# Optimization experiments

Hardware: AMD Instinct MI355X
Metric: run time of the kernel (lower is better)

The kernel has to match this reference:

```python
import jax, jax.numpy as jnp
import numpy as np

B, S, D, H = 4, 2048, 1024, 16
DH = D // H


def setup_inputs() -> dict:
    key = jax.random.key(0)
    ks = jax.random.split(key, 12)
    s = 0.02
    inp = {
        "q": jax.random.normal(ks[0], (B, S, D), jnp.float32),
        "k": jax.random.normal(ks[1], (B, S, D), jnp.float32),
        "v": jax.random.normal(ks[2], (B, S, D), jnp.float32),
        # causal mask, broadcastable over batch and heads (mask==0 -> -1e9)
        "mask": jnp.tril(jnp.ones((S, S), jnp.int32))[None, None, :, :],
        "wq": jax.random.normal(ks[3], (D, D), jnp.float32) * s,
        "bq": jnp.zeros((D,), jnp.float32),
        "wk": jax.random.normal(ks[4], (D, D), jnp.float32) * s,
        "bk": jnp.zeros((D,), jnp.float32),
        "wv": jax.random.normal(ks[5], (D, D), jnp.float32) * s,
        "bv": jnp.zeros((D,), jnp.float32),
        "wo": jax.random.normal(ks[6], (D, D), jnp.float32) * s,
        "bo": jnp.zeros((D,), jnp.float32),
    }
    return inp


def reference(q, k, v, mask, wq, bq, wk, bk, wv, bv, wo, bo):
    # linear projections (torch Linear: x @ W^T + b)
    qh = (q @ wq.T + bq).reshape(B, S, H, DH).transpose(0, 2, 1, 3)  # [B,H,S,DH]
    kh = (k @ wk.T + bk).reshape(B, S, H, DH).transpose(0, 2, 1, 3)
    vh = (v @ wv.T + bv).reshape(B, S, H, DH).transpose(0, 2, 1, 3)
    scale = 1.0 / jnp.sqrt(jnp.float32(DH))
    score = jnp.einsum("bhqd,bhkd->bhqk", qh, kh) * scale  # [B,H,S,S]
    score = jnp.where(mask == 0, jnp.float32(-1e9), score)
    attn = jax.nn.softmax(score, axis=-1)
    ctx = jnp.einsum("bhqk,bhkd->bhqd", attn, vh)  # [B,H,S,DH]
    ctx = ctx.transpose(0, 2, 1, 3).reshape(B, S, D)
    return ctx @ wo.T + bo
```

## Files before the change

kernel.cpp:

```cpp
#include <hip/hip_runtime.h>
#include <hip/hip_bf16.h>

#define NB 4
#define NS 2048
#define ND 1024
#define NH 16
#define NDH 64
#define E_ 8388608
#define W_ 1048576

typedef __attribute__((ext_vector_type(8))) __bf16 bf16x8;
typedef __attribute__((ext_vector_type(4))) float f32x4;
typedef __attribute__((ext_vector_type(2))) unsigned int u32x2;
typedef unsigned short us16;
typedef unsigned int u32;

__device__ __forceinline__ unsigned short f2bf(float f) {
  union { float f; unsigned u; } v; v.f = f;
  unsigned r = v.u + 0x7FFFu + ((v.u >> 16) & 1u);
  return (unsigned short)(r >> 16);
}

typedef const __attribute__((address_space(1))) unsigned int* gas_t;
typedef __attribute__((address_space(3))) unsigned int* las_t;
__device__ __forceinline__ void gl2lds16(const void* g, void* l) {
  __builtin_amdgcn_global_load_lds((gas_t)g, (las_t)l, 16, 0, 0);
}

__global__ __launch_bounds__(256) void conv_bf16(
    const float* __restrict__ q, const float* __restrict__ k, const float* __restrict__ v,
    const float* __restrict__ wq, const float* __restrict__ wk, const float* __restrict__ wv,
    const float* __restrict__ wo,
    us16* __restrict__ qb, us16* __restrict__ kb, us16* __restrict__ vb,
    us16* __restrict__ wqb, us16* __restrict__ wkb, us16* __restrict__ wvb,
    us16* __restrict__ wob)
{
  int b = blockIdx.x;
  int seg, off;
  if (b < 24576) { seg = b >> 13; off = b & 8191; }
  else { b -= 24576; seg = 3 + (b >> 10); off = b & 1023; }
  const float* s; us16* d;
  switch (seg) {
    case 0: s = q;  d = qb;  break;
    case 1: s = k;  d = kb;  break;
    case 2: s = v;  d = vb;  break;
    case 3: s = wq; d = wqb; break;
    case 4: s = wk; d = wkb; break;
    case 5: s = wv; d = wvb; break;
    default: s = wo; d = wob; break;
  }
  size_t idx = ((size_t)off * 256 + threadIdx.x) * 4;
  float4 f = *(const float4*)(s + idx);
  ushort4 u;
  u.x = f2bf(f.x); u.y = f2bf(f.y); u.z = f2bf(f.z); u.w = f2bf(f.w);
  *(ushort4*)(d + idx) = u;
}

__global__ __launch_bounds__(256, 3) void gemm_proj3(
    const us16* __restrict__ A0, const us16* __restrict__ A1, const us16* __restrict__ A2,
    const us16* __restrict__ W0, const us16* __restrict__ W1, const us16* __restrict__ W2,
    const float* __restrict__ b0, const float* __restrict__ b1, const float* __restrict__ b2,
    us16* __restrict__ o0, us16* __restrict__ o1, us16* __restrict__ o2,
    float qscale, int s0, int s1, int s2)
{
  const int seg = (blockIdx.z == 0) ? s0 : (blockIdx.z == 1) ? s1 : s2;
  const us16* A  = (blockIdx.z == 0) ? A0 : (blockIdx.z == 1) ? A1 : A2;
  const us16* Wt = (blockIdx.z == 0) ? W0 : (blockIdx.z == 1) ? W1 : W2;
  const float* bias = (blockIdx.z == 0) ? b0 : (blockIdx.z == 1) ? b1 : b2;
  us16* out = (blockIdx.z == 0) ? o0 : (blockIdx.z == 1) ? o1 : o2;
  const float scale = (seg == 0) ? qscale : 1.0f;

  __shared__ us16 As[128][64];
  __shared__ us16 Bs[128][64];
  const int tid = threadIdx.x;
  const int lane = tid & 63;
  const int w = tid >> 6;
  const int l15 = lane & 15, quad = lane >> 4;
  const int sw = l15 & 7;
  const int rowBase = blockIdx.x * 128, colBase = blockIdx.y * 128;
  const int srow = w * 32 + (lane >> 3);
  const int cu = (lane & 7) ^ ((lane >> 3) & 7);
  const us16* ga = A  + (size_t)(rowBase + srow) * ND + cu * 8;
  const us16* gb = Wt + (size_t)(colBase + srow) * ND + cu * 8;
  const int wr = (w >> 1) * 64, wc = (w & 1) * 64;

  f32x4 acc[4][4] = {};
  for (int kt = 0; kt < ND; kt += 64) {
    __syncthreads();
    #pragma unroll
    for (int c = 0; c < 4; ++c) {
      gl2lds16(ga + kt + c * 8 * ND, &As[w * 32 + c * 8][0]);
      gl2lds16(gb + kt + c * 8 * ND, &Bs[w * 32 + c * 8][0]);
    }
    __syncthreads();
    #pragma unroll
    for (int ks = 0; ks < 2; ++ks) {
      bf16x8 af[4], bfr[4];
      #pragma unroll
      for (int i = 0; i < 4; ++i)
        af[i]  = *(const bf16x8*)&As[wr + i * 16 + l15][((ks * 4 + quad) ^ sw) * 8];
      #pragma unroll
      for (int j = 0; j < 4; ++j)
        bfr[j] = *(const bf16x8*)&Bs[wc + j * 16 + l15][((ks * 4 + quad) ^ sw) * 8];
      #pragma unroll
      for (int i = 0; i < 4; ++i)
        #pragma unroll
        for (int j = 0; j < 4; ++j)
          acc[i][j] = __builtin_amdgcn_mfma_f32_16x16x32_bf16(af[i], bfr[j], acc[i][j], 0, 0, 0);
    }
  }

  if (seg < 2) {
    #pragma unroll
    for (int i = 0; i < 4; ++i) {
      #pragma unroll
      for (int j = 0; j < 4; ++j) {
        int colg = colBase + wc + j * 16 + l15;
        float bval = bias[colg];
        #pragma unroll
        for (int r = 0; r < 4; ++r) {
          int rowg = rowBase + wr + i * 16 + quad * 4 + r;
          out[(size_t)rowg * ND + colg] = f2bf((acc[i][j][r] + bval) * scale);
        }
      }
    }
  } else {
    #pragma unroll
    for (int i = 0; i < 4; ++i) {
      #pragma unroll
      for (int j = 0; j < 4; ++j) {
        int colg = colBase + wc + j * 16 + l15;
        float bval = bias[colg];
        int h_ = colg >> 6, d_ = colg & 63;
        int rowg0 = rowBase + wr + i * 16 + quad * 4;
        int b_ = rowg0 >> 11, sr0 = rowg0 & (NS - 1);
        ushort4 vv;
        vv.x = f2bf(acc[i][j][0] + bval);
        vv.y = f2bf(acc[i][j][1] + bval);
        vv.z = f2bf(acc[i][j][2] + bval);
        vv.w = f2bf(acc[i][j][3] + bval);
        *(ushort4*)(out + ((size_t)(b_ * NH + h_) * NDH + d_) * NS + sr0) = vv;
      }
    }
  }
}

__global__ __launch_bounds__(256, 2) void attn(
    const us16* __restrict__ Qh, const us16* __restrict__ Kh,
    const us16* __restrict__ Vht, us16* __restrict__ ctx)
{
  __shared__ us16 Ks[2][128][64];
  __shared__ us16 Vts[2][64][128];
  __shared__ us16 Ps[4][32][32];
  us16* Qsta = &Vts[1][0][0];

  const int bh = blockIdx.x & 63;
  const int pr = blockIdx.x >> 6;
  const int b_ = bh >> 4, h_ = bh & 15;
  const int tid = threadIdx.x, lane = tid & 63, w = tid >> 6;
  const int l15 = lane & 15, quad = lane >> 4;
  const int sw = l15 & 7;
  const int lr8 = lane >> 3;
  const int cu = (lane & 7) ^ (lr8 & 7);
  const int vr = lane >> 4;
  const int vs = lane & 15;
  const int cs0 = (vs & 8) | ((vs & 7) ^ vr);
  const int cs1 = (vs & 8) | ((vs & 7) ^ (vr | 4));

  bf16x8 ones;
  #pragma unroll
  for (int i = 0; i < 8; ++i) ones[i] = (__bf16)1.0f;

  const us16* gk  = Kh  + ((size_t)b_ * NS + w * 32 + lr8) * ND + h_ * NDH + cu * 8;
  const us16* gv0 = Vht + ((size_t)bh * NDH + w * 16 + vr) * NS + cs0 * 8;
  const us16* gv1 = Vht + ((size_t)bh * NDH + w * 16 + 4 + vr) * NS + cs1 * 8;

  for (int pass = 0; pass < 2; ++pass) {
    const int tq = pass ? (15 - pr) : pr;
    const int qb0 = tq * 128;
    const int nt = tq + 1;
    const int qw = qb0 + w * 32;

    __syncthreads();
    {
      const us16* gq = Qh + ((size_t)b_ * NS + qb0 + w * 32 + lr8) * ND + h_ * NDH + cu * 8;
      #pragma unroll
      for (int u = 0; u < 4; ++u)
        gl2lds16(gq + (size_t)u * 8 * ND, Qsta + (w * 32 + u * 8) * 64);
    }
    #pragma unroll
    for (int u = 0; u < 4; ++u)
      gl2lds16(gk + (size_t)(u * 8) * ND, &Ks[0][w * 32 + u * 8][0]);
    gl2lds16(gv0,          &Vts[0][w * 16][0]);
    gl2lds16(gv1,          &Vts[0][w * 16 + 4][0]);
    gl2lds16(gv0 + 8 * NS, &Vts[0][w * 16 + 8][0]);
    gl2lds16(gv1 + 8 * NS, &Vts[0][w * 16 + 12][0]);
    __syncthreads();
    bf16x8 bq[2][2];
    #pragma unroll
    for (int ntl = 0; ntl < 2; ++ntl)
      #pragma unroll
      for (int c = 0; c < 2; ++c)
        bq[ntl][c] = *(const bf16x8*)(Qsta + (w * 32 + ntl * 16 + l15) * 64 +
                                      (((c * 4 + quad) ^ sw) * 8));

    f32x4 o[2][4] = {};
    f32x4 o_l[2] = {};

    for (int it = 0; it < nt; ++it) {
      const int kb = it * 128;
      const int cur = it & 1;
      __syncthreads();
      if (it + 1 < nt) {
        const int nxt = cur ^ 1;
        const int kn = kb + 128;
        #pragma unroll
        for (int u = 0; u < 4; ++u)
          gl2lds16(gk + (size_t)(kn + u * 8) * ND, &Ks[nxt][w * 32 + u * 8][0]);
        gl2lds16(gv0 + kn,          &Vts[nxt][w * 16][0]);
        gl2lds16(gv1 + kn,          &Vts[nxt][w * 16 + 4][0]);
        gl2lds16(gv0 + kn + 8 * NS, &Vts[nxt][w * 16 + 8][0]);
        gl2lds16(gv1 + kn + 8 * NS, &Vts[nxt][w * 16 + 12][0]);
      }
      #pragma unroll
      for (int h2 = 0; h2 < 4; ++h2) {
        const int keyb0 = kb + h2 * 32;
        if (keyb0 > qw + 31) continue;
        const bool full = (keyb0 + 31 <= qw);
        f32x4 s[2][2];
        __builtin_amdgcn_s_setprio(1);
        #pragma unroll
        for (int mt = 0; mt < 2; ++mt) {
          bf16x8 ak0 = *(const bf16x8*)&Ks[cur][h2 * 32 + mt * 16 + l15][(quad ^ sw) * 8];
          bf16x8 ak1 = *(const bf16x8*)&Ks[cur][h2 * 32 + mt * 16 + l15][((4 + quad) ^ sw) * 8];
          #pragma unroll
          for (int ntl = 0; ntl < 2; ++ntl) {
            f32x4 t = {};
            t = __builtin_amdgcn_mfma_f32_16x16x32_bf16(ak0, bq[ntl][0], t, 0, 0, 0);
            t = __builtin_amdgcn_mfma_f32_16x16x32_bf16(ak1, bq[ntl][1], t, 0, 0, 0);
            s[mt][ntl] = t;
          }
        }
        __builtin_amdgcn_s_setprio(0);
        #pragma unroll
        for (int mt = 0; mt < 2; ++mt)
          #pragma unroll
          for (int ntl = 0; ntl < 2; ++ntl) {
            u32 u[4];
            if (full) {
              #pragma unroll
              for (int r = 0; r < 4; ++r)
                u[r] = __float_as_uint(__builtin_amdgcn_exp2f(s[mt][ntl][r]));
            } else {
              const int keyb = keyb0 + mt * 16 + quad * 4;
              const int qg = qw + ntl * 16 + l15;
              #pragma unroll
              for (int r = 0; r < 4; ++r) {
                float p = (keyb + r <= qg) ? __builtin_amdgcn_exp2f(s[mt][ntl][r]) : 0.f;
                u[r] = __float_as_uint(p);
              }
            }
            u32 lo = (u[0] >> 16) | (u[1] & 0xffff0000u);
            u32 hi = (u[2] >> 16) | (u[3] & 0xffff0000u);
            int uswz = (mt * 2 + (quad >> 1)) ^ (l15 & 3);
            *(u32x2*)&Ps[w][ntl * 16 + l15][uswz * 8 + (quad & 1) * 4] = (u32x2){lo, hi};
          }
        bf16x8 bv[4];
        #pragma unroll
        for (int n = 0; n < 4; ++n)
          bv[n] = *(const bf16x8*)&Vts[cur][n * 16 + l15][((h2 * 4 + quad) ^ sw) * 8];
        __builtin_amdgcn_s_setprio(1);
        #pragma unroll
        for (int ntl = 0; ntl < 2; ++ntl) {
          bf16x8 ap = *(const bf16x8*)&Ps[w][ntl * 16 + l15][(quad ^ (l15 & 3)) * 8];
          o_l[ntl] = __builtin_amdgcn_mfma_f32_16x16x32_bf16(ap, ones, o_l[ntl], 0, 0, 0);
          #pragma unroll
          for (int n = 0; n < 4; ++n)
            o[ntl][n] = __builtin_amdgcn_mfma_f32_16x16x32_bf16(ap, bv[n], o[ntl][n], 0, 0, 0);
        }
        __builtin_amdgcn_s_setprio(0);
      }
    }

    #pragma unroll
    for (int ntl = 0; ntl < 2; ++ntl) {
      #pragma unroll
      for (int r = 0; r < 4; ++r) {
        float inv = __builtin_amdgcn_rcpf(o_l[ntl][r]);
        int qg = qb0 + w * 32 + ntl * 16 + quad * 4 + r;
        us16* dst = ctx + ((size_t)b_ * NS + qg) * ND + h_ * NDH;
        #pragma unroll
        for (int n = 0; n < 4; ++n)
          dst[n * 16 + l15] = f2bf(o[ntl][n][r] * inv);
      }
    }
  }
}

__global__ __launch_bounds__(256, 3) void gemm_out(
    const us16* __restrict__ A, const us16* __restrict__ Wt,
    const float* __restrict__ bias, float* __restrict__ out)
{
  __shared__ us16 As[128][64];
  __shared__ us16 Bs[128][64];
  const int tid = threadIdx.x;
  const int lane = tid & 63;
  const int w = tid >> 6;
  const int l15 = lane & 15, quad = lane >> 4;
  const int sw = l15 & 7;
  const int rowBase = blockIdx.x * 128, colBase = blockIdx.y * 128;
  const int srow = w * 32 + (lane >> 3);
  const int cu = (lane & 7) ^ ((lane >> 3) & 7);
  const us16* ga = A  + (size_t)(rowBase + srow) * ND + cu * 8;
  const us16* gb = Wt + (size_t)(colBase + srow) * ND + cu * 8;
  const int wr = (w >> 1) * 64, wc = (w & 1) * 64;

  f32x4 acc[4][4] = {};
  for (int kt = 0; kt < ND; kt += 64) {
    __syncthreads();
    #pragma unroll
    for (int c = 0; c < 4; ++c) {
      gl2lds16(ga + kt + c * 8 * ND, &As[w * 32 + c * 8][0]);
      gl2lds16(gb + kt + c * 8 * ND, &Bs[w * 32 + c * 8][0]);
    }
    __syncthreads();
    #pragma unroll
    for (int ks = 0; ks < 2; ++ks) {
      bf16x8 af[4], bfr[4];
      #pragma unroll
      for (int i = 0; i < 4; ++i)
        af[i]  = *(const bf16x8*)&As[wr + i * 16 + l15][((ks * 4 + quad) ^ sw) * 8];
      #pragma unroll
      for (int j = 0; j < 4; ++j)
        bfr[j] = *(const bf16x8*)&Bs[wc + j * 16 + l15][((ks * 4 + quad) ^ sw) * 8];
      #pragma unroll
      for (int i = 0; i < 4; ++i)
        #pragma unroll
        for (int j = 0; j < 4; ++j)
          acc[i][j] = __builtin_amdgcn_mfma_f32_16x16x32_bf16(af[i], bfr[j], acc[i][j], 0, 0, 0);
    }
  }

  #pragma unroll
  for (int i = 0; i < 4; ++i) {
    #pragma unroll
    for (int j = 0; j < 4; ++j) {
      int colg = colBase + wc + j * 16 + l15;
      float bval = bias[colg];
      #pragma unroll
      for (int r = 0; r < 4; ++r) {
        int rowg = rowBase + wr + i * 16 + quad * 4 + r;
        out[(size_t)rowg * ND + colg] = acc[i][j][r] + bval;
      }
    }
  }
}

extern "C" void kernel_launch(void* const* d_in, const int* in_sizes, int n_in,
                              void* d_out, int out_size, void* d_ws, size_t ws_size,
                              hipStream_t stream) {
  const float* q  = (const float*)d_in[0];
  const float* k  = (const float*)d_in[1];
  const float* v  = (const float*)d_in[2];
  const float* wq = (const float*)d_in[4];
  const float* bq_ = (const float*)d_in[5];
  const float* wk = (const float*)d_in[6];
  const float* bk_ = (const float*)d_in[7];
  const float* wv = (const float*)d_in[8];
  const float* bv_ = (const float*)d_in[9];
  const float* wo = (const float*)d_in[10];
  const float* bo_ = (const float*)d_in[11];

  us16* ws = (us16*)d_ws;
  us16* qb  = ws;
  us16* kb  = ws + (size_t)E_;
  us16* vb  = ws + (size_t)2 * E_;
  us16* wqb = ws + (size_t)3 * E_;
  us16* wkb = wqb + W_;
  us16* wvb = wkb + W_;
  us16* wob = wvb + W_;
  us16* KhF = wob + W_;
  us16* ctx = vb;
  us16* Vht = (us16*)d_out;
  us16* Qh  = (us16*)d_out + (size_t)E_;

  const float qscale = 0.125f * 1.44269504088896340736f;
  const bool fused = ws_size >= ((size_t)4 * E_ + 4 * W_) * 2;

  conv_bf16<<<28672, 256, 0, stream>>>(q, k, v, wq, wk, wv, wo,
                                       qb, kb, vb, wqb, wkb, wvb, wob);
  if (fused) {
    gemm_proj3<<<dim3(64, 8, 3), 256, 0, stream>>>(
        qb, kb, vb, wqb, wkb, wvb, bq_, bk_, bv_, Qh, KhF, Vht, qscale, 0, 1, 2);
    attn<<<512, 256, 0, stream>>>(Qh, KhF, Vht, ctx);
  } else {
    gemm_proj3<<<dim3(64, 8, 2), 256, 0, stream>>>(
        qb, vb, vb, wqb, wvb, wvb, bq_, bv_, bv_, Qh, Vht, Vht, qscale, 0, 2, 2);
    gemm_proj3<<<dim3(64, 8, 1), 256, 0, stream>>>(
        kb, kb, kb, wkb, wkb, wkb, bk_, bk_, bk_, qb, qb, qb, qscale, 1, 1, 1);
    attn<<<512, 256, 0, stream>>>(Qh, qb, Vht, ctx);
  }
  gemm_out<<<dim3(64, 8), 256, 0, stream>>>(ctx, wob, bo_, (float*)d_out);
}
```

Measured before the change: 305.4 us.

## Use 8-wave 256x128 GEMM tiles with 4-stage LDS ring pipeline

Replaces the projection and output GEMMs with 512-thread blocks computing 256x128 tiles, a K step of 32, and a 4-deep LDS buffer ring. Global-to-LDS loads are issued three stages ahead with explicit vmcnt waits and one barrier per step, replacing the two syncthreads per 64-K step. MFMA sections are raised in priority with s_setprio. The aim is to hide load latency behind matrix math and cut barrier stalls, at the cost of more LDS per block (96 KB) and lower block-level occupancy.

Result: slower. 326.4 us (+6.9%).

```diff
diff --git a/kernel.cpp b/kernel.cpp
--- a/kernel.cpp
+++ b/kernel.cpp
@@ -56,7 +56,44 @@
   *(ushort4*)(d + idx) = u;
 }
 
-__global__ __launch_bounds__(256, 3) void gemm_proj3(
+#define STG(bi, kt) { \
+    gl2lds16(ga + (kt),             &As[bi][w * 32][0]); \
+    gl2lds16(ga + (kt) + 16 * ND,   &As[bi][w * 32 + 16][0]); \
+    gl2lds16(gb + (kt),             &Bs[bi][w * 16][0]); }
+
+#define BARX() { __builtin_amdgcn_s_barrier(); \
+                 __builtin_amdgcn_sched_barrier(0); \
+                 asm volatile("" ::: "memory"); }
+
+#define GEMM8_PIPE() \
+  f32x4 acc[4][4] = {}; \
+  STG(0, 0) STG(1, 32) STG(2, 64) \
+  asm volatile("s_waitcnt vmcnt(6)" ::: "memory"); \
+  BARX() \
+  _Pragma("unroll") \
+  for (int t = 0; t < 32; ++t) { \
+    if (t + 3 < 32) STG((t + 3) & 3, (t + 3) * 32) \
+    bf16x8 af[4], bfr[4]; \
+    _Pragma("unroll") \
+    for (int i = 0; i < 4; ++i) \
+      af[i] = *(const bf16x8*)&As[t & 3][wm * 64 + i * 16 + l15][(quad ^ (l15 & 3)) * 8]; \
+    _Pragma("unroll") \
+    for (int j = 0; j < 4; ++j) \
+      bfr[j] = *(const bf16x8*)&Bs[t & 3][wn * 64 + j * 16 + l15][(quad ^ (l15 & 3)) * 8]; \
+    __builtin_amdgcn_s_setprio(1); \
+    _Pragma("unroll") \
+    for (int i = 0; i < 4; ++i) \
+      _Pragma("unroll") \
+      for (int j = 0; j < 4; ++j) \
+        acc[i][j] = __builtin_amdgcn_mfma_f32_16x16x32_bf16(af[i], bfr[j], acc[i][j], 0, 0, 0); \
+    __builtin_amdgcn_s_setprio(0); \
+    if (t < 29)       asm volatile("s_waitcnt vmcnt(6)" ::: "memory"); \
+    else if (t == 29) asm volatile("s_waitcnt vmcnt(3)" ::: "memory"); \
+    else if (t == 30) asm volatile("s_waitcnt vmcnt(0)" ::: "memory"); \
+    if (t < 31) BARX() \
+  }
+
+__global__ __launch_bounds__(512, 2) void gemm_proj8(
     const us16* __restrict__ A0, const us16* __restrict__ A1, const us16* __restrict__ A2,
     const us16* __restrict__ W0, const us16* __restrict__ W1, const us16* __restrict__ W2,
     const float* __restrict__ b0, const float* __restrict__ b1, const float* __restrict__ b2,
@@ -70,46 +107,22 @@
   us16* out = (blockIdx.z == 0) ? o0 : (blockIdx.z == 1) ? o1 : o2;
   const float scale = (seg == 0) ? qscale : 1.0f;
 
-  __shared__ us16 As[128][64];
-  __shared__ us16 Bs[128][64];
+  __shared__ us16 As[4][256][32];
+  __shared__ us16 Bs[4][128][32];
   const int tid = threadIdx.x;
   const int lane = tid & 63;
   const int w = tid >> 6;
   const int l15 = lane & 15, quad = lane >> 4;
-  const int sw = l15 & 7;
-  const int rowBase = blockIdx.x * 128, colBase = blockIdx.y * 128;
-  const int srow = w * 32 + (lane >> 3);
-  const int cu = (lane & 7) ^ ((lane >> 3) & 7);
-  const us16* ga = A  + (size_t)(rowBase + srow) * ND + cu * 8;
-  const us16* gb = Wt + (size_t)(colBase + srow) * ND + cu * 8;
-  const int wr = (w >> 1) * 64, wc = (w & 1) * 64;
-
-  f32x4 acc[4][4] = {};
-  for (int kt = 0; kt < ND; kt += 64) {
-    __syncthreads();
-    #pragma unroll
-    for (int c = 0; c < 4; ++c) {
-      gl2lds16(ga + kt + c * 8 * ND, &As[w * 32 + c * 8][0]);
-      gl2lds16(gb + kt + c * 8 * ND, &Bs[w * 32 + c * 8][0]);
-    }
-    __syncthreads();
-    #pragma unroll
-    for (int ks = 0; ks < 2; ++ks) {
-      bf16x8 af[4], bfr[4];
-      #pragma unroll
-      for (int i = 0; i < 4; ++i)
-        af[i]  = *(const bf16x8*)&As[wr + i * 16 + l15][((ks * 4 + quad) ^ sw) * 8];
-      #pragma unroll
-      for (int j = 0; j < 4; ++j)
-        bfr[j] = *(const bf16x8*)&Bs[wc + j * 16 + l15][((ks * 4 + quad) ^ sw) * 8];
-      #pragma unroll
-      for (int i = 0; i < 4; ++i)
-        #pragma unroll
-        for (int j = 0; j < 4; ++j)
-          acc[i][j] = __builtin_amdgcn_mfma_f32_16x16x32_bf16(af[i], bfr[j], acc[i][j], 0, 0, 0);
-    }
-  }
-
+  const int lr4 = lane >> 2;
+  const int cu4 = (lane & 3) ^ (lr4 & 3);
+  const int wm = w >> 1, wn = w & 1;
+  const int rowBase = blockIdx.x * 256, colBase = blockIdx.y * 128;
+  const us16* ga = A  + (size_t)(rowBase + w * 32 + lr4) * ND + cu4 * 8;
+  const us16* gb = Wt + (size_t)(colBase + w * 16 + lr4) * ND + cu4 * 8;
+
+  GEMM8_PIPE()
+
+  const int wr = wm * 64, wc = wn * 64;
   if (seg < 2) {
     #pragma unroll
     for (int i = 0; i < 4; ++i) {
@@ -140,6 +153,41 @@
         vv.z = f2bf(acc[i][j][2] + bval);
         vv.w = f2bf(acc[i][j][3] + bval);
         *(ushort4*)(out + ((size_t)(b_ * NH + h_) * NDH + d_) * NS + sr0) = vv;
+      }
+    }
+  }
+}
+
+__global__ __launch_bounds__(512, 2) void gemm_out8(
+    const us16* __restrict__ A, const us16* __restrict__ Wt,
+    const float* __restrict__ bias, float* __restrict__ out)
+{
+  __shared__ us16 As[4][256][32];
+  __shared__ us16 Bs[4][128][32];
+  const int tid = threadIdx.x;
+  const int lane = tid & 63;
+  const int w = tid >> 6;
+  const int l15 = lane & 15, quad = lane >> 4;
+  const int lr4 = lane >> 2;
+  const int cu4 = (lane & 3) ^ (lr4 & 3);
+  const int wm = w >> 1, wn = w & 1;
+  const int rowBase = blockIdx.x * 256, colBase = blockIdx.y * 128;
+  const us16* ga = A  + (size_t)(rowBase + w * 32 + lr4) * ND + cu4 * 8;
+  const us16* gb = Wt + (size_t)(colBase + w * 16 + lr4) * ND + cu4 * 8;
+
+  GEMM8_PIPE()
+
+  const int wr = wm * 64, wc = wn * 64;
+  #pragma unroll
+  for (int i = 0; i < 4; ++i) {
+    #pragma unroll
+    for (int j = 0; j < 4; ++j) {
+      int colg = colBase + wc + j * 16 + l15;
+      float bval = bias[colg];
+      #pragma unroll
+      for (int r = 0; r < 4; ++r) {
+        int rowg = rowBase + wr + i * 16 + quad * 4 + r;
+        out[(size_t)rowg * ND + colg] = acc[i][j][r] + bval;
       }
     }
   }
@@ -297,65 +345,6 @@
   }
 }
 
-__global__ __launch_bounds__(256, 3) void gemm_out(
-    const us16* __restrict__ A, const us16* __restrict__ Wt,
-    const float* __restrict__ bias, float* __restrict__ out)
-{
-  __shared__ us16 As[128][64];
-  __shared__ us16 Bs[128][64];
-  const int tid = threadIdx.x;
-  const int lane = tid & 63;
-  const int w = tid >> 6;
-  const int l15 = lane & 15, quad = lane >> 4;
-  const int sw = l15 & 7;
-  const int rowBase = blockIdx.x * 128, colBase = blockIdx.y * 128;
-  const int srow = w * 32 + (lane >> 3);
-  const int cu = (lane & 7) ^ ((lane >> 3) & 7);
-  const us16* ga = A  + (size_t)(rowBase + srow) * ND + cu * 8;
-  const us16* gb = Wt + (size_t)(colBase + srow) * ND + cu * 8;
-  const int wr = (w >> 1) * 64, wc = (w & 1) * 64;
-
-  f32x4 acc[4][4] = {};
-  for (int kt = 0; kt < ND; kt += 64) {
-    __syncthreads();
-    #pragma unroll
-    for (int c = 0; c < 4; ++c) {
-      gl2lds16(ga + kt + c * 8 * ND, &As[w * 32 + c * 8][0]);
-      gl2lds16(gb + kt + c * 8 * ND, &Bs[w * 32 + c * 8][0]);
-    }
-    __syncthreads();
-    #pragma unroll
-    for (int ks = 0; ks < 2; ++ks) {
-      bf16x8 af[4], bfr[4];
-      #pragma unroll
-      for (int i = 0; i < 4; ++i)
-        af[i]  = *(const bf16x8*)&As[wr + i * 16 + l15][((ks * 4 + quad) ^ sw) * 8];
-      #pragma unroll
-      for (int j = 0; j < 4; ++j)
-        bfr[j] = *(const bf16x8*)&Bs[wc + j * 16 + l15][((ks * 4 + quad) ^ sw) * 8];
-      #pragma unroll
-      for (int i = 0; i < 4; ++i)
-        #pragma unroll
-        for (int j = 0; j < 4; ++j)
-          acc[i][j] = __builtin_amdgcn_mfma_f32_16x16x32_bf16(af[i], bfr[j], acc[i][j], 0, 0, 0);
-    }
-  }
-
-  #pragma unroll
-  for (int i = 0; i < 4; ++i) {
-    #pragma unroll
-    for (int j = 0; j < 4; ++j) {
-      int colg = colBase + wc + j * 16 + l15;
-      float bval = bias[colg];
-      #pragma unroll
-      for (int r = 0; r < 4; ++r) {
-        int rowg = rowBase + wr + i * 16 + quad * 4 + r;
-        out[(size_t)rowg * ND + colg] = acc[i][j][r] + bval;
-      }
-    }
-  }
-}
-
 extern "C" void kernel_launch(void* const* d_in, const int* in_sizes, int n_in,
                               void* d_out, int out_size, void* d_ws, size_t ws_size,
                               hipStream_t stream) {
@@ -390,15 +379,15 @@
   conv_bf16<<<28672, 256, 0, stream>>>(q, k, v, wq, wk, wv, wo,
                                        qb, kb, vb, wqb, wkb, wvb, wob);
   if (fused) {
-    gemm_proj3<<<dim3(64, 8, 3), 256, 0, stream>>>(
+    gemm_proj8<<<dim3(32, 8, 3), 512, 0, stream>>>(
         qb, kb, vb, wqb, wkb, wvb, bq_, bk_, bv_, Qh, KhF, Vht, qscale, 0, 1, 2);
     attn<<<512, 256, 0, stream>>>(Qh, KhF, Vht, ctx);
   } else {
-    gemm_proj3<<<dim3(64, 8, 2), 256, 0, stream>>>(
+    gemm_proj8<<<dim3(32, 8, 2), 512, 0, stream>>>(
         qb, vb, vb, wqb, wvb, wvb, bq_, bv_, bv_, Qh, Vht, Vht, qscale, 0, 2, 2);
-    gemm_proj3<<<dim3(64, 8, 1), 256, 0, stream>>>(
+    gemm_proj8<<<dim3(32, 8, 1), 512, 0, stream>>>(
         kb, kb, kb, wkb, wkb, wkb, bk_, bk_, bk_, qb, qb, qb, qscale, 1, 1, 1);
     attn<<<512, 256, 0, stream>>>(Qh, qb, Vht, ctx);
   }
-  gemm_out<<<dim3(64, 8), 256, 0, stream>>>(ctx, wob, bo_, (float*)d_out);
-}
+  gemm_out8<<<dim3(32, 8), 512, 0, stream>>>(ctx, wob, bo_, (float*)d_out);
+}
```

## Split attention block across eight waves with sixteen query rows each

Applied to the files above, without the earlier changes.

The attention kernel moves from 4 waves handling 32 query rows each to 8 waves (512 threads) handling 16 query rows each. The K/V tile loads are shared across the doubled wave count, and per-wave accumulators and the P scratch shrink. The aim is more waves in flight to hide LDS and MFMA latency and to reduce register pressure. In exchange, each wave re-reads the K and V fragments from LDS for half as many query rows, which raises LDS traffic per FLOP, and barrier cost grows with more waves.

Result: faster. 297.8 us (-2.5%).

```diff
diff --git a/kernel.cpp b/kernel.cpp
--- a/kernel.cpp
+++ b/kernel.cpp
@@ -145,13 +145,13 @@
   }
 }
 
-__global__ __launch_bounds__(256, 2) void attn(
+__global__ __launch_bounds__(512, 2) void attn(
     const us16* __restrict__ Qh, const us16* __restrict__ Kh,
     const us16* __restrict__ Vht, us16* __restrict__ ctx)
 {
   __shared__ us16 Ks[2][128][64];
   __shared__ us16 Vts[2][64][128];
-  __shared__ us16 Ps[4][32][32];
+  __shared__ us16 Ps[8][16][32];
   us16* Qsta = &Vts[1][0][0];
 
   const int bh = blockIdx.x & 63;
@@ -171,41 +171,34 @@
   #pragma unroll
   for (int i = 0; i < 8; ++i) ones[i] = (__bf16)1.0f;
 
-  const us16* gk  = Kh  + ((size_t)b_ * NS + w * 32 + lr8) * ND + h_ * NDH + cu * 8;
-  const us16* gv0 = Vht + ((size_t)bh * NDH + w * 16 + vr) * NS + cs0 * 8;
-  const us16* gv1 = Vht + ((size_t)bh * NDH + w * 16 + 4 + vr) * NS + cs1 * 8;
+  const us16* gk  = Kh  + ((size_t)b_ * NS + w * 16 + lr8) * ND + h_ * NDH + cu * 8;
+  const us16* gv0 = Vht + ((size_t)bh * NDH + w * 8 + vr) * NS + cs0 * 8;
+  const us16* gv1 = Vht + ((size_t)bh * NDH + w * 8 + 4 + vr) * NS + cs1 * 8;
 
   for (int pass = 0; pass < 2; ++pass) {
     const int tq = pass ? (15 - pr) : pr;
     const int qb0 = tq * 128;
     const int nt = tq + 1;
-    const int qw = qb0 + w * 32;
+    const int qw = qb0 + w * 16;
 
     __syncthreads();
     {
-      const us16* gq = Qh + ((size_t)b_ * NS + qb0 + w * 32 + lr8) * ND + h_ * NDH + cu * 8;
-      #pragma unroll
-      for (int u = 0; u < 4; ++u)
-        gl2lds16(gq + (size_t)u * 8 * ND, Qsta + (w * 32 + u * 8) * 64);
-    }
-    #pragma unroll
-    for (int u = 0; u < 4; ++u)
-      gl2lds16(gk + (size_t)(u * 8) * ND, &Ks[0][w * 32 + u * 8][0]);
-    gl2lds16(gv0,          &Vts[0][w * 16][0]);
-    gl2lds16(gv1,          &Vts[0][w * 16 + 4][0]);
-    gl2lds16(gv0 + 8 * NS, &Vts[0][w * 16 + 8][0]);
-    gl2lds16(gv1 + 8 * NS, &Vts[0][w * 16 + 12][0]);
-    __syncthreads();
-    bf16x8 bq[2][2];
-    #pragma unroll
-    for (int ntl = 0; ntl < 2; ++ntl)
-      #pragma unroll
-      for (int c = 0; c < 2; ++c)
-        bq[ntl][c] = *(const bf16x8*)(Qsta + (w * 32 + ntl * 16 + l15) * 64 +
-                                      (((c * 4 + quad) ^ sw) * 8));
-
-    f32x4 o[2][4] = {};
-    f32x4 o_l[2] = {};
+      const us16* gq = Qh + ((size_t)b_ * NS + qb0 + w * 16 + lr8) * ND + h_ * NDH + cu * 8;
+      gl2lds16(gq,                    Qsta + (w * 16) * 64);
+      gl2lds16(gq + (size_t)8 * ND,   Qsta + (w * 16 + 8) * 64);
+    }
+    gl2lds16(gk,            &Ks[0][w * 16][0]);
+    gl2lds16(gk + 8 * ND,   &Ks[0][w * 16 + 8][0]);
+    gl2lds16(gv0,           &Vts[0][w * 8][0]);
+    gl2lds16(gv1,           &Vts[0][w * 8 + 4][0]);
+    __syncthreads();
+    bf16x8 bq[2];
+    #pragma unroll
+    for (int c = 0; c < 2; ++c)
+      bq[c] = *(const bf16x8*)(Qsta + (w * 16 + l15) * 64 + (((c * 4 + quad) ^ sw) * 8));
+
+    f32x4 o[4] = {};
+    f32x4 o_l = {};
 
     for (int it = 0; it < nt; ++it) {
       const int kb = it * 128;
@@ -214,85 +207,73 @@
       if (it + 1 < nt) {
         const int nxt = cur ^ 1;
         const int kn = kb + 128;
-        #pragma unroll
-        for (int u = 0; u < 4; ++u)
-          gl2lds16(gk + (size_t)(kn + u * 8) * ND, &Ks[nxt][w * 32 + u * 8][0]);
-        gl2lds16(gv0 + kn,          &Vts[nxt][w * 16][0]);
-        gl2lds16(gv1 + kn,          &Vts[nxt][w * 16 + 4][0]);
-        gl2lds16(gv0 + kn + 8 * NS, &Vts[nxt][w * 16 + 8][0]);
-        gl2lds16(gv1 + kn + 8 * NS, &Vts[nxt][w * 16 + 12][0]);
+        gl2lds16(gk + (size_t)kn * ND,        &Ks[nxt][w * 16][0]);
+        gl2lds16(gk + (size_t)(kn + 8) * ND,  &Ks[nxt][w * 16 + 8][0]);
+        gl2lds16(gv0 + kn,                    &Vts[nxt][w * 8][0]);
+        gl2lds16(gv1 + kn,                    &Vts[nxt][w * 8 + 4][0]);
       }
       #pragma unroll
       for (int h2 = 0; h2 < 4; ++h2) {
         const int keyb0 = kb + h2 * 32;
-        if (keyb0 > qw + 31) continue;
+        if (keyb0 > qw + 15) continue;
         const bool full = (keyb0 + 31 <= qw);
-        f32x4 s[2][2];
+        f32x4 s[2];
         __builtin_amdgcn_s_setprio(1);
         #pragma unroll
         for (int mt = 0; mt < 2; ++mt) {
           bf16x8 ak0 = *(const bf16x8*)&Ks[cur][h2 * 32 + mt * 16 + l15][(quad ^ sw) * 8];
           bf16x8 ak1 = *(const bf16x8*)&Ks[cur][h2 * 32 + mt * 16 + l15][((4 + quad) ^ sw) * 8];
-          #pragma unroll
-          for (int ntl = 0; ntl < 2; ++ntl) {
-            f32x4 t = {};
-            t = __builtin_amdgcn_mfma_f32_16x16x32_bf16(ak0, bq[ntl][0], t, 0, 0, 0);
-            t = __builtin_amdgcn_mfma_f32_16x16x32_bf16(ak1, bq[ntl][1], t, 0, 0, 0);
-            s[mt][ntl] = t;
-          }
+          f32x4 t = {};
+          t = __builtin_amdgcn_mfma_f32_16x16x32_bf16(ak0, bq[0], t, 0, 0, 0);
+          t = __builtin_amdgcn_mfma_f32_16x16x32_bf16(ak1, bq[1], t, 0, 0, 0);
+          s[mt] = t;
         }
         __builtin_amdgcn_s_setprio(0);
         #pragma unroll
-        for (int mt = 0; mt < 2; ++mt)
-          #pragma unroll
-          for (int ntl = 0; ntl < 2; ++ntl) {
-            u32 u[4];
-            if (full) {
-              #pragma unroll
-              for (int r = 0; r < 4; ++r)
-                u[r] = __float_as_uint(__builtin_amdgcn_exp2f(s[mt][ntl][r]));
-            } else {
-              const int keyb = keyb0 + mt * 16 + quad * 4;
-              const int qg = qw + ntl * 16 + l15;
-              #pragma unroll
-              for (int r = 0; r < 4; ++r) {
-                float p = (keyb + r <= qg) ? __builtin_amdgcn_exp2f(s[mt][ntl][r]) : 0.f;
-                u[r] = __float_as_uint(p);
-              }
+        for (int mt = 0; mt < 2; ++mt) {
+          u32 u[4];
+          if (full) {
+            #pragma unroll
+            for (int r = 0; r < 4; ++r)
+              u[r] = __float_as_uint(__builtin_amdgcn_exp2f(s[mt][r]));
+          } else {
+            const int keyb = keyb0 + mt * 16 + quad * 4;
+            const int qg = qw + l15;
+            #pragma unroll
+            for (int r = 0; r < 4; ++r) {
+              float p = (keyb + r <= qg) ? __builtin_amdgcn_exp2f(s[mt][r]) : 0.f;
+              u[r] = __float_as_uint(p);
             }
-            u32 lo = (u[0] >> 16) | (u[1] & 0xffff0000u);
-            u32 hi = (u[2] >> 16) | (u[3] & 0xffff0000u);
-            int uswz = (mt * 2 + (quad >> 1)) ^ (l15 & 3);
-            *(u32x2*)&Ps[w][ntl * 16 + l15][uswz * 8 + (quad & 1) * 4] = (u32x2){lo, hi};
           }
+          u32 lo = (u[0] >> 16) | (u[1] & 0xffff0000u);
+          u32 hi = (u[2] >> 16) | (u[3] & 0xffff0000u);
+          int uswz = (mt * 2 + (quad >> 1)) ^ (l15 & 3);
+          *(u32x2*)&Ps[w][l15][uswz * 8 + (quad & 1) * 4] = (u32x2){lo, hi};
+        }
         bf16x8 bv[4];
         #pragma unroll
         for (int n = 0; n < 4; ++n)
           bv[n] = *(const bf16x8*)&Vts[cur][n * 16 + l15][((h2 * 4 + quad) ^ sw) * 8];
         __builtin_amdgcn_s_setprio(1);
-        #pragma unroll
-        for (int ntl = 0; ntl < 2; ++ntl) {
-          bf16x8 ap = *(const bf16x8*)&Ps[w][ntl * 16 + l15][(quad ^ (l15 & 3)) * 8];
-          o_l[ntl] = __builtin_amdgcn_mfma_f32_16x16x32_bf16(ap, ones, o_l[ntl], 0, 0, 0);
+        {
+          bf16x8 ap = *(const bf16x8*)&Ps[w][l15][(quad ^ (l15 & 3)) * 8];
+          o_l = __builtin_amdgcn_mfma_f32_16x16x32_bf16(ap, ones, o_l, 0, 0, 0);
           #pragma unroll
           for (int n = 0; n < 4; ++n)
-            o[ntl][n] = __builtin_amdgcn_mfma_f32_16x16x32_bf16(ap, bv[n], o[ntl][n], 0, 0, 0);
+            o[n] = __builtin_amdgcn_mfma_f32_16x16x32_bf16(ap, bv[n], o[n], 0, 0, 0);
         }
         __builtin_amdgcn_s_setprio(0);
       }
     }
 
     #pragma unroll
-    for (int ntl = 0; ntl < 2; ++ntl) {
-      #pragma unroll
-      for (int r = 0; r < 4; ++r) {
-        float inv = __builtin_amdgcn_rcpf(o_l[ntl][r]);
-        int qg = qb0 + w * 32 + ntl * 16 + quad * 4 + r;
-        us16* dst = ctx + ((size_t)b_ * NS + qg) * ND + h_ * NDH;
-        #pragma unroll
-        for (int n = 0; n < 4; ++n)
-          dst[n * 16 + l15] = f2bf(o[ntl][n][r] * inv);
-      }
+    for (int r = 0; r < 4; ++r) {
+      float inv = __builtin_amdgcn_rcpf(o_l[r]);
+      int qg = qb0 + w * 16 + quad * 4 + r;
+      us16* dst = ctx + ((size_t)b_ * NS + qg) * ND + h_ * NDH;
+      #pragma unroll
+      for (int n = 0; n < 4; ++n)
+        dst[n * 16 + l15] = f2bf(o[n][r] * inv);
     }
   }
 }
@@ -392,13 +373,13 @@
   if (fused) {
     gemm_proj3<<<dim3(64, 8, 3), 256, 0, stream>>>(
         qb, kb, vb, wqb, wkb, wvb, bq_, bk_, bv_, Qh, KhF, Vht, qscale, 0, 1, 2);
-    attn<<<512, 256, 0, stream>>>(Qh, KhF, Vht, ctx);
+    attn<<<512, 512, 0, stream>>>(Qh, KhF, Vht, ctx);
   } else {
     gemm_proj3<<<dim3(64, 8, 2), 256, 0, stream>>>(
         qb, vb, vb, wqb, wvb, wvb, bq_, bv_, bv_, Qh, Vht, Vht, qscale, 0, 2, 2);
     gemm_proj3<<<dim3(64, 8, 1), 256, 0, stream>>>(
         kb, kb, kb, wkb, wkb, wkb, bk_, bk_, bk_, qb, qb, qb, qscale, 1, 1, 1);
-    attn<<<512, 256, 0, stream>>>(Qh, qb, Vht, ctx);
+    attn<<<512, 512, 0, stream>>>(Qh, qb, Vht, ctx);
   }
   gemm_out<<<dim3(64, 8), 256, 0, stream>>>(ctx, wob, bo_, (float*)d_out);
 }
```
